# Kernel tuning notes

Hardware: AMD Instinct MI355X
Metric: run time of the kernel (lower is better)

## Reference

```python
import jax, jax.numpy as jnp
import numpy as np

N, E, G = 50000, 400000, 500
H, C, IN, ED = 4, 64, 9, 3
NEG = 0.2   # LeakyReLU negative slope (PyG GATv2 default)
EPS = 1e-5  # BatchNorm eps


def _gatv2(x, src, dst, ea, Wl, bl, Wr, We, att, bias):
    # PyG GATv2Conv, concat=False (mean over heads), eval mode (no dropout)
    xl = (x @ Wl + bl).reshape(-1, H, C)   # source transform  [N,H,C]
    xr = (x @ Wr).reshape(-1, H, C)        # target transform  [N,H,C]
    ee = (ea @ We).reshape(-1, H, C)       # edge transform    [E,H,C]
    m = xl[src] + xr[dst] + ee             # [E,H,C]
    s = jnp.einsum('ehc,hc->eh', jax.nn.leaky_relu(m, NEG), att)  # [E,H]
    smax = jax.ops.segment_max(s, dst, num_segments=N)
    ex = jnp.exp(s - smax[dst])
    den = jax.ops.segment_sum(ex, dst, num_segments=N)
    alpha = ex / den[dst]                  # segment softmax over in-edges of dst
    out = jax.ops.segment_sum(xl[src] * alpha[:, :, None], dst, num_segments=N)
    return out.mean(axis=1) + bias         # [N,C]


def _bn(x, g, b, mu, var):
    return (x - mu) * (g * jax.lax.rsqrt(var + EPS)) + b


def setup_inputs() -> dict:
    key = jax.random.key(0)
    ks = jax.random.split(key, 32)
    f = lambda k, s: (jax.random.normal(k, s, jnp.float32) * 0.1)
    inp = dict(
        x=jax.random.normal(ks[0], (N, IN), jnp.float32),
        edge_index=jax.random.randint(ks[1], (2, E), 0, N),
        batch=jnp.sort(jax.random.randint(ks[2], (N,), 0, G)),
        edge_attr=jax.random.normal(ks[3], (E, ED), jnp.float32),
        # input head conv (in=9)
        W0l=f(ks[4], (IN, H * C)), b0l=f(ks[5], (H * C,)),
        W0r=f(ks[6], (IN, H * C)), W0e=f(ks[7], (ED, H * C)),
        a0=f(ks[8], (H, C)), c0=f(ks[9], (C,)),
        # 3 residual conv layers (in=64), stacked
        Wl=f(ks[10], (3, C, H * C)), bl=f(ks[11], (3, H * C)),
        Wr=f(ks[12], (3, C, H * C)), We=f(ks[13], (3, ED, H * C)),
        a=f(ks[14], (3, H, C)), cb=f(ks[15], (3, C)),
        # 4 batchnorms (eval mode running stats)
        bn_g=jnp.ones((4, C), jnp.float32) + f(ks[16], (4, C)),
        bn_b=f(ks[17], (4, C)),
        bn_m=f(ks[18], (4, C)),
        bn_v=jnp.ones((4, C), jnp.float32),
        # output MLP head
        Wo1=f(ks[19], (C, C // 2)), bo1=f(ks[20], (C // 2,)),
        Wo2=f(ks[21], (C // 2, 1)), bo2=f(ks[22], (1,)),
    )
    return inp


def reference(x, edge_index, batch, edge_attr,
              W0l, b0l, W0r, W0e, a0, c0,
              Wl, bl, Wr, We, a, cb,
              bn_g, bn_b, bn_m, bn_v,
              Wo1, bo1, Wo2, bo2):
    src, dst = edge_index[0], edge_index[1]
    h = _gatv2(x, src, dst, edge_attr, W0l, b0l, W0r, W0e, a0, c0)
    h = jax.nn.elu(_bn(h, bn_g[0], bn_b[0], bn_m[0], bn_v[0]))
    for i in range(3):
        z = _gatv2(h, src, dst, edge_attr, Wl[i], bl[i], Wr[i], We[i], a[i], cb[i])
        z = jax.nn.elu(_bn(z, bn_g[i + 1], bn_b[i + 1], bn_m[i + 1], bn_v[i + 1]))
        h = h + z
    # global mean pool over graphs
    cnt = jax.ops.segment_sum(jnp.ones((N,), h.dtype), batch, num_segments=G)
    pooled = jax.ops.segment_sum(h, batch, num_segments=G) / jnp.maximum(cnt, 1.0)[:, None]
    hid = jax.nn.elu(pooled @ Wo1 + bo1)
    return hid @ Wo2 + bo2  # [G,1]
```

## Files before the change

kernel.cpp:

```cpp
#include <hip/hip_runtime.h>
#include <hip/hip_fp16.h>
#include <math.h>

typedef _Float16 h8 __attribute__((ext_vector_type(8)));
typedef float f4 __attribute__((ext_vector_type(4)));

__global__ __launch_bounds__(256) void count_kernel(const int* __restrict__ dst,
                                                    int* __restrict__ deg, int E) {
    int e = blockIdx.x * 256 + threadIdx.x;
    if (e < E) atomicAdd(&deg[dst[e]], 1);
}

#define SCAN_TPB 256
#define SCAN_VPT 4
#define SCAN_ELEMS (SCAN_TPB * SCAN_VPT)

__global__ __launch_bounds__(256) void scan_phase1(const int* __restrict__ deg,
                                                   int* __restrict__ bsum, int n) {
    __shared__ int sh[SCAN_TPB];
    int base = blockIdx.x * SCAN_ELEMS + threadIdx.x * SCAN_VPT;
    int s = 0;
#pragma unroll
    for (int j = 0; j < SCAN_VPT; j++) { int i = base + j; if (i < n) s += deg[i]; }
    sh[threadIdx.x] = s;
    __syncthreads();
    for (int off = 128; off; off >>= 1) {
        if (threadIdx.x < (unsigned)off) sh[threadIdx.x] += sh[threadIdx.x + off];
        __syncthreads();
    }
    if (threadIdx.x == 0) bsum[blockIdx.x] = sh[0];
}

__global__ __launch_bounds__(256) void scan_phase2(int* __restrict__ bsum, int nb,
                                                   int* __restrict__ rowptr, int n) {
    __shared__ int sh[256];
    int v = (threadIdx.x < (unsigned)nb) ? bsum[threadIdx.x] : 0;
    sh[threadIdx.x] = v;
    __syncthreads();
    for (int off = 1; off < 256; off <<= 1) {
        int t = (threadIdx.x >= (unsigned)off) ? sh[threadIdx.x - off] : 0;
        __syncthreads();
        sh[threadIdx.x] += t;
        __syncthreads();
    }
    if (threadIdx.x < (unsigned)nb) bsum[threadIdx.x] = sh[threadIdx.x] - v;
    if (threadIdx.x == 0) rowptr[n] = sh[255];
}

__global__ __launch_bounds__(256) void scan_phase3(const int* __restrict__ deg,
                                                   const int* __restrict__ bsum,
                                                   int* __restrict__ rowptr,
                                                   int* __restrict__ cursor, int n) {
    __shared__ int sh[SCAN_TPB];
    int tid = threadIdx.x;
    int base = blockIdx.x * SCAN_ELEMS + tid * SCAN_VPT;
    int v[SCAN_VPT];
    int s = 0;
#pragma unroll
    for (int j = 0; j < SCAN_VPT; j++) { int i = base + j; v[j] = (i < n) ? deg[i] : 0; s += v[j]; }
    sh[tid] = s;
    __syncthreads();
    for (int off = 1; off < SCAN_TPB; off <<= 1) {
        int t = (tid >= off) ? sh[tid - off] : 0;
        __syncthreads();
        sh[tid] += t;
        __syncthreads();
    }
    int ex = sh[tid] - s + bsum[blockIdx.x];
#pragma unroll
    for (int j = 0; j < SCAN_VPT; j++) {
        int i = base + j;
        if (i < n) { rowptr[i] = ex; cursor[i] = ex; ex += v[j]; }
    }
}

__global__ __launch_bounds__(256) void scatter_kernel(const int* __restrict__ src,
                                                      const int* __restrict__ dst,
                                                      const float* __restrict__ ea,
                                                      int* __restrict__ cursor,
                                                      float4* __restrict__ csr4, int E) {
    int e = blockIdx.x * 256 + threadIdx.x;
    if (e < E) {
        int d = dst[e];
        int pos = atomicAdd(&cursor[d], 1);
        size_t eb3 = (size_t)e * 3;
        csr4[pos] = make_float4(__int_as_float(src[e]), ea[eb3], ea[eb3 + 1], ea[eb3 + 2]);
    }
}

__global__ __launch_bounds__(256) void bnprep_kernel(const float* __restrict__ c0,
                                                     const float* __restrict__ cb,
                                                     const float* __restrict__ bng,
                                                     const float* __restrict__ bnb,
                                                     const float* __restrict__ bnm,
                                                     const float* __restrict__ bnv,
                                                     float* __restrict__ epi) {
    int t = threadIdx.x;
    int l = t >> 6, c = t & 63;
    float s = bng[l * 64 + c] * rsqrtf(bnv[l * 64 + c] + 1e-5f);
    float bias = (l == 0) ? c0[c] : cb[(l - 1) * 64 + c];
    epi[l * 128 + c] = 0.25f * s;
    epi[l * 128 + 64 + c] = (bias - bnm[l * 64 + c]) * s + bnb[l * 64 + c];
}

__global__ __launch_bounds__(256) void gstart_kernel(const int* __restrict__ batch,
                                                     int* __restrict__ gstart,
                                                     int Nn, int Gg) {
    int n = blockIdx.x * 256 + threadIdx.x;
    if (n >= Nn) return;
    int b = batch[n];
    int prev = (n == 0) ? -1 : batch[n - 1];
    for (int g = prev + 1; g <= b; g++) gstart[g] = n;
    if (n == Nn - 1)
        for (int g = b + 1; g <= Gg; g++) gstart[g] = Nn;
}

__global__ __launch_bounds__(256) void wprep_kernel(const float* __restrict__ W0l,
                                                    const float* __restrict__ W0r,
                                                    const float* __restrict__ Wl,
                                                    const float* __restrict__ Wr,
                                                    __half* __restrict__ Wp) {
    int t = blockIdx.x * 256 + threadIdx.x;
    int layer = t >> 12;
    int r = t & 4095;
    int lane = r & 63;
    int ks = (r >> 6) & 1;
    int gct = r >> 7;
    int K = (layer == 0) ? 9 : 64;
    const float* Wsrc;
    if (layer == 0) Wsrc = (gct < 16) ? W0l : W0r;
    else            Wsrc = ((gct < 16) ? Wl : Wr) + (size_t)(layer - 1) * 64 * 256;
    int cl = ((gct & 15) << 4) + (lane & 15);
    int k0 = (ks << 5) + ((lane >> 4) << 3);
    __half vals[8] __attribute__((aligned(16)));
#pragma unroll
    for (int j = 0; j < 8; j++) {
        int k = k0 + j;
        vals[j] = __float2half_rn((k < K) ? Wsrc[(size_t)k * 256 + cl] : 0.f);
    }
    *(uint4*)(Wp + (size_t)t * 8) = *(const uint4*)vals;
}

template <int K>
__global__ __launch_bounds__(256) void gemm2_mfma_kernel(const float* __restrict__ xin,
                                                         const __half* __restrict__ Wp,
                                                         const float* __restrict__ bl,
                                                         __half* __restrict__ xl,
                                                         __half* __restrict__ xr, int Nn) {
    constexpr int NKS = (K > 32) ? 2 : 1;
    constexpr int KP = NKS * 32;
    __shared__ __align__(16) float shx[32][KP + 4];
    int tid = threadIdx.x;
    int lane = tid & 63;
    int wv = tid >> 6;
    int nb = blockIdx.x * 32;
    int l15 = lane & 15;
    int lg = lane >> 4;

    if (K != KP) {
        for (int q = tid; q < 32 * KP; q += 256) shx[q / KP][q % KP] = 0.f;
        __syncthreads();
    }
    if (K == 64) {
        for (int q = tid; q < 32 * 16; q += 256) {
            int r = q >> 4, c4 = q & 15;
            int node = nb + r;
            float4 v = (node < Nn) ? *(const float4*)(xin + (size_t)node * 64 + c4 * 4)
                                   : make_float4(0.f, 0.f, 0.f, 0.f);
            *(float4*)&shx[r][c4 * 4] = v;
        }
    } else {
        for (int q = tid; q < 32 * K; q += 256) {
            int r = q / K, c = q - r * K;
            int node = nb + r;
            shx[r][c] = (node < Nn) ? xin[(size_t)node * K + c] : 0.f;
        }
    }
    __syncthreads();

    h8 afr[8][NKS];
#pragma unroll
    for (int i = 0; i < 8; i++) {
        int gct = wv * 8 + i;
#pragma unroll
        for (int ks = 0; ks < NKS; ks++)
            afr[i][ks] = *(const h8*)(Wp + (((size_t)(gct * 2 + ks)) * 64 + lane) * 8);
    }
    h8 bfr[2][NKS];
#pragma unroll
    for (int nt = 0; nt < 2; nt++) {
        int row = nt * 16 + l15;
#pragma unroll
        for (int ks = 0; ks < NKS; ks++) {
            int k0 = ks * 32 + lg * 8;
            float4 f0 = *(const float4*)&shx[row][k0];
            float4 f1 = *(const float4*)&shx[row][k0 + 4];
            h8 b;
            b[0] = (_Float16)f0.x; b[1] = (_Float16)f0.y;
            b[2] = (_Float16)f0.z; b[3] = (_Float16)f0.w;
            b[4] = (_Float16)f1.x; b[5] = (_Float16)f1.y;
            b[6] = (_Float16)f1.z; b[7] = (_Float16)f1.w;
            bfr[nt][ks] = b;
        }
    }
    f4 acc[8][2];
#pragma unroll
    for (int i = 0; i < 8; i++) {
        int gct = wv * 8 + i;
        f4 ini;
        if (gct < 16) {
            float4 b4 = *(const float4*)(bl + (gct << 4) + (lg << 2));
            ini[0] = b4.x; ini[1] = b4.y; ini[2] = b4.z; ini[3] = b4.w;
        } else {
            ini[0] = 0.f; ini[1] = 0.f; ini[2] = 0.f; ini[3] = 0.f;
        }
        acc[i][0] = ini;
        acc[i][1] = ini;
    }
#pragma unroll
    for (int i = 0; i < 8; i++)
#pragma unroll
        for (int nt = 0; nt < 2; nt++)
#pragma unroll
            for (int ks = 0; ks < NKS; ks++)
                acc[i][nt] = __builtin_amdgcn_mfma_f32_16x16x32_f16(
                    afr[i][ks], bfr[nt][ks], acc[i][nt], 0, 0, 0);
#pragma unroll
    for (int i = 0; i < 8; i++) {
        int gct = wv * 8 + i;
        __half* outp = (gct < 16) ? xl : xr;
        int cl = ((gct & 15) << 4) + (lg << 2);
#pragma unroll
        for (int nt = 0; nt < 2; nt++) {
            int node = nb + nt * 16 + l15;
            if (node < Nn) {
                __half h4[4] __attribute__((aligned(8)));
                h4[0] = __float2half_rn(acc[i][nt][0]);
                h4[1] = __float2half_rn(acc[i][nt][1]);
                h4[2] = __float2half_rn(acc[i][nt][2]);
                h4[3] = __float2half_rn(acc[i][nt][3]);
                *(uint2*)(outp + (size_t)node * 256 + cl) = *(const uint2*)h4;
            }
        }
    }
}

#define EB 6

#define GISSUE(S, ibase)                                                               \
    {                                                                                  \
        _Pragma("unroll") for (int j = 0; j < EB; j++) {                               \
            int idx = (ibase) + j;                                                     \
            if (idx < end) {                                                           \
                float4 ce = csr4[idx];                  \
                cey##S[j] = ce.y; cez##S[j] = ce.z; cew##S[j] = ce.w;                  \
                int sn = __float_as_int(ce.x);                                         \
                xpk##S[j] = *(const uint2*)(xl + ((size_t)sn << 8) + (lane << 2));     \
            } else {                                                                   \
                cey##S[j] = 0.f; cez##S[j] = 0.f; cew##S[j] = 0.f;                     \
                xpk##S[j] = make_uint2(0u, 0u);                                        \
            }                                                                          \
        }                                                                              \
    }

#define GCOMPUTE(S, ibase)                                                             \
    {                                                                                  \
        float p[EB];                                                                   \
        _Pragma("unroll") for (int j = 0; j < EB; j++) {                               \
            int idx = (ibase) + j;                                                     \
            if (idx < end) {                                                           \
                float2 f0 = __half22float2(*(const __half2*)&xpk##S[j].x);             \
                float2 f1 = __half22float2(*(const __half2*)&xpk##S[j].y);             \
                float tx = fmaf(cey##S[j], we0.x,                                      \
                             fmaf(cez##S[j], we1.x, fmaf(cew##S[j], we2.x, xr0.x)))    \
                           + f0.x;                                                     \
                float ty = fmaf(cey##S[j], we0.y,                                      \
                             fmaf(cez##S[j], we1.y, fmaf(cew##S[j], we2.y, xr0.y)))    \
                           + f0.y;                                                     \
                float tz = fmaf(cey##S[j], we0.z,                                      \
                             fmaf(cez##S[j], we1.z, fmaf(cew##S[j], we2.z, xr1.x)))    \
                           + f1.x;                                                     \
                float tw = fmaf(cey##S[j], we0.w,                                      \
                             fmaf(cez##S[j], we1.w, fmaf(cew##S[j], we2.w, xr1.y)))    \
                           + f1.y;                                                     \
                float pp = tx * (tx > 0.f ? attv.x : att02.x);                         \
                pp = fmaf(ty, (ty > 0.f ? attv.y : att02.y), pp);                      \
                pp = fmaf(tz, (tz > 0.f ? attv.z : att02.z), pp);                      \
                pp = fmaf(tw, (tw > 0.f ? attv.w : att02.w), pp);                      \
                p[j] = pp;                                                             \
            } else p[j] = -INFINITY;                                                   \
        }                                                                              \
        _Pragma("unroll") for (int off = 1; off < 16; off <<= 1) {                     \
            _Pragma("unroll") for (int j = 0; j < EB; j++) p[j] += __shfl_xor(p[j], off); \
        }                                                                              \
        _Pragma("unroll") for (int j = 0; j < EB; j++) {                               \
            float wv2 = __expf(p[j]);                                                  \
            float2 f0 = __half22float2(*(const __half2*)&xpk##S[j].x);                 \
            float2 f1 = __half22float2(*(const __half2*)&xpk##S[j].y);                 \
            acc.x = fmaf(wv2, f0.x, acc.x);                                            \
            acc.y = fmaf(wv2, f0.y, acc.y);                                            \
            acc.z = fmaf(wv2, f1.x, acc.z);                                            \
            acc.w = fmaf(wv2, f1.y, acc.w);                                            \
            l_run += wv2;                                                              \
        }                                                                              \
    }

__global__ __launch_bounds__(256) void gat_kernel(const __half* __restrict__ xl,
                                                  const __half* __restrict__ xr,
                                                  const float* __restrict__ We,
                                                  const float* __restrict__ att,
                                                  const float* __restrict__ epi,
                                                  const int* __restrict__ rowptr,
                                                  const float4* __restrict__ csr4,
                                                  float* __restrict__ hout,
                                                  const float* __restrict__ hres,
                                                  int Nn) {
    int tid = threadIdx.x;
    int lane = tid & 63;
    int w = __builtin_amdgcn_readfirstlane(tid >> 6);
    int wave = blockIdx.x * 4 + w;
    int nwaves = gridDim.x * 4;

    float4 we0 = *(const float4*)&We[lane * 4];
    float4 we1 = *(const float4*)&We[256 + lane * 4];
    float4 we2 = *(const float4*)&We[512 + lane * 4];
    float4 attv = *(const float4*)&att[lane * 4];
    float4 att02 = make_float4(0.2f * attv.x, 0.2f * attv.y, 0.2f * attv.z, 0.2f * attv.w);
    float4 eA = *(const float4*)&epi[(lane & 15) * 4];
    float4 eB4 = *(const float4*)&epi[64 + (lane & 15) * 4];

    int d = wave;
    if (d >= Nn) return;
    int beg = rowptr[d];
    int end = rowptr[d + 1];
    uint2 xrp = *(const uint2*)(xr + ((size_t)d << 8) + (lane << 2));

    uint2 xpkA[EB], xpkB[EB];
    float ceyA[EB], cezA[EB], cewA[EB], ceyB[EB], cezB[EB], cewB[EB];

    while (d < Nn) {
        int dn = d + nwaves;
        int begn = 0, endn = 0;
        uint2 xrpn = make_uint2(0u, 0u);
        if (dn < Nn) {
            begn = rowptr[dn];
            endn = rowptr[dn + 1];
            xrpn = *(const uint2*)(xr + ((size_t)dn << 8) + (lane << 2));
        }
        float2 xr0 = __half22float2(*(const __half2*)&xrp.x);
        float2 xr1 = __half22float2(*(const __half2*)&xrp.y);

        float l_run = 0.f;
        float4 acc = make_float4(0.f, 0.f, 0.f, 0.f);

        int i = beg;
        if (i < end) {
            GISSUE(A, i);
            for (;;) {
                int nx = i + EB;
                if (nx < end) GISSUE(B, nx);
                GCOMPUTE(A, i);
                i = nx;
                if (i >= end) break;
                nx = i + EB;
                if (nx < end) GISSUE(A, nx);
                GCOMPUTE(B, i);
                i = nx;
                if (i >= end) break;
            }
        }
        float inv = (end > beg) ? 1.f / l_run : 0.f;
        float4 o = make_float4(acc.x * inv, acc.y * inv, acc.z * inv, acc.w * inv);
#pragma unroll
        for (int off = 16; off < 64; off <<= 1) {
            o.x += __shfl_xor(o.x, off);
            o.y += __shfl_xor(o.y, off);
            o.z += __shfl_xor(o.z, off);
            o.w += __shfl_xor(o.w, off);
        }
        if (lane < 16) {
            float vx = fmaf(o.x, eA.x, eB4.x);
            float vy = fmaf(o.y, eA.y, eB4.y);
            float vz = fmaf(o.z, eA.z, eB4.z);
            float vw = fmaf(o.w, eA.w, eB4.w);
            vx = vx > 0.f ? vx : expm1f(vx);
            vy = vy > 0.f ? vy : expm1f(vy);
            vz = vz > 0.f ? vz : expm1f(vz);
            vw = vw > 0.f ? vw : expm1f(vw);
            if (hres) {
                float4 r4 = *(const float4*)&hres[((size_t)d << 6) + (lane << 2)];
                vx += r4.x; vy += r4.y; vz += r4.z; vw += r4.w;
            }
            *(float4*)&hout[((size_t)d << 6) + (lane << 2)] = make_float4(vx, vy, vz, vw);
        }
        d = dn; beg = begn; end = endn; xrp = xrpn;
    }
}

__global__ __launch_bounds__(256) void pool_kernel(const float* __restrict__ h,
                                                   const int* __restrict__ gstart,
                                                   float* __restrict__ pooled, int Gg) {
    __shared__ float red[4][64];
    int g = blockIdx.x;
    int tid = threadIdx.x;
    int lane = tid & 63, w = tid >> 6;
    int gs = gstart[g], ge = gstart[g + 1];
    float s = 0.f;
    for (int n = gs + w; n < ge; n += 4) s += h[((size_t)n << 6) + lane];
    red[w][lane] = s;
    __syncthreads();
    if (tid < 64) {
        float tot = red[0][tid] + red[1][tid] + red[2][tid] + red[3][tid];
        float c = fmaxf((float)(ge - gs), 1.f);
        pooled[((size_t)g << 6) + tid] = tot / c;
    }
}

__global__ __launch_bounds__(64) void head_kernel(const float* __restrict__ pooled,
                                                  const float* __restrict__ Wo1,
                                                  const float* __restrict__ bo1,
                                                  const float* __restrict__ Wo2,
                                                  const float* __restrict__ bo2,
                                                  float* __restrict__ out, int Gg) {
    int g = blockIdx.x;
    int t = threadIdx.x;
    __shared__ float sp[64];
    sp[t] = pooled[(size_t)g * 64 + t];
    __syncthreads();
    float hid = 0.f;
    if (t < 32) {
        hid = bo1[t];
        for (int k = 0; k < 64; k++) hid += sp[k] * Wo1[k * 32 + t];
        hid = hid > 0.f ? hid : expm1f(hid);
        hid *= Wo2[t];
    }
#pragma unroll
    for (int off = 32; off; off >>= 1) hid += __shfl_xor(hid, off);
    if (t == 0) out[g] = hid + bo2[0];
}

extern "C" void kernel_launch(void* const* d_in, const int* in_sizes, int n_in,
                              void* d_out, int out_size, void* d_ws, size_t ws_size,
                              hipStream_t stream) {
    const float* x   = (const float*)d_in[0];
    const int*   ei  = (const int*)d_in[1];
    const int*   bat = (const int*)d_in[2];
    const float* ea  = (const float*)d_in[3];
    const float* W0l = (const float*)d_in[4];
    const float* b0l = (const float*)d_in[5];
    const float* W0r = (const float*)d_in[6];
    const float* W0e = (const float*)d_in[7];
    const float* a0  = (const float*)d_in[8];
    const float* c0  = (const float*)d_in[9];
    const float* Wl  = (const float*)d_in[10];
    const float* bl  = (const float*)d_in[11];
    const float* Wr  = (const float*)d_in[12];
    const float* We  = (const float*)d_in[13];
    const float* a   = (const float*)d_in[14];
    const float* cb  = (const float*)d_in[15];
    const float* bng = (const float*)d_in[16];
    const float* bnb = (const float*)d_in[17];
    const float* bnm = (const float*)d_in[18];
    const float* bnv = (const float*)d_in[19];
    const float* Wo1 = (const float*)d_in[20];
    const float* bo1 = (const float*)d_in[21];
    const float* Wo2 = (const float*)d_in[22];
    const float* bo2 = (const float*)d_in[23];

    int Nn = in_sizes[2];
    int Ee = in_sizes[1] / 2;
    int Gg = out_size;
    const int* srcv = ei;
    const int* dstv = ei + Ee;

    char* w = (char*)d_ws;
    auto alloc = [&](size_t bytes) {
        char* p = w;
        w += (bytes + 255) & ~(size_t)255;
        return p;
    };
    __half* xlb    = (__half*)alloc((size_t)Nn * 256 * 2);
    __half* xrb    = (__half*)alloc((size_t)Nn * 256 * 2);
    float*  hbuf   = (float*)alloc((size_t)Nn * 64 * 4);
    int*    deg    = (int*)alloc((size_t)Nn * 4);
    int*    rowptr = (int*)alloc((size_t)(Nn + 1) * 4);
    int*    cursor = (int*)alloc((size_t)Nn * 4);
    float4* csr4   = (float4*)alloc((size_t)Ee * 16);
    float*  pooled = (float*)alloc((size_t)Gg * 64 * 4);
    int*    gstart = (int*)alloc((size_t)(Gg + 1) * 4);
    int*    bsum   = (int*)alloc(256 * 4);
    float*  epi    = (float*)alloc(4 * 128 * 4);
    __half* Wp     = (__half*)alloc((size_t)4 * 32768 * 2);

    int nscan = (Nn + SCAN_ELEMS - 1) / SCAN_ELEMS;

    hipMemsetAsync(deg, 0, (size_t)Nn * 4, stream);
    count_kernel<<<(Ee + 255) / 256, 256, 0, stream>>>(dstv, deg, Ee);
    scan_phase1<<<nscan, 256, 0, stream>>>(deg, bsum, Nn);
    scan_phase2<<<1, 256, 0, stream>>>(bsum, nscan, rowptr, Nn);
    scan_phase3<<<nscan, 256, 0, stream>>>(deg, bsum, rowptr, cursor, Nn);
    scatter_kernel<<<(Ee + 255) / 256, 256, 0, stream>>>(srcv, dstv, ea, cursor, csr4, Ee);
    bnprep_kernel<<<1, 256, 0, stream>>>(c0, cb, bng, bnb, bnm, bnv, epi);
    wprep_kernel<<<64, 256, 0, stream>>>(W0l, W0r, Wl, Wr, Wp);
    gstart_kernel<<<(Nn + 255) / 256, 256, 0, stream>>>(bat, gstart, Nn, Gg);

    int gatg = 2048;
    int gemg = (Nn + 31) / 32;

    gemm2_mfma_kernel<9><<<gemg, 256, 0, stream>>>(x, Wp, b0l, xlb, xrb, Nn);
    gat_kernel<<<gatg, 256, 0, stream>>>(xlb, xrb, W0e, a0, epi,
                                         rowptr, csr4, hbuf, nullptr, Nn);
    for (int i = 0; i < 3; i++) {
        gemm2_mfma_kernel<64><<<gemg, 256, 0, stream>>>(
            hbuf, Wp + (size_t)(i + 1) * 32768, bl + (size_t)i * 256, xlb, xrb, Nn);
        gat_kernel<<<gatg, 256, 0, stream>>>(
            xlb, xrb, We + (size_t)i * 768, a + (size_t)i * 256, epi + (size_t)(i + 1) * 128,
            rowptr, csr4, hbuf, hbuf, Nn);
    }

    pool_kernel<<<Gg, 256, 0, stream>>>(hbuf, gstart, pooled, Gg);
    head_kernel<<<Gg, 64, 0, stream>>>(pooled, Wo1, bo1, Wo2, bo2, (float*)d_out, Gg);
}
```

Measured before the change: 425.8 us.

## Balance GAT node ranges across waves by edge count using rowptr binary search

Adds a small kernel that splits the destination nodes into 8192 contiguous ranges holding roughly equal numbers of edges, found by binary search over rowptr. Each GAT wave now walks its own contiguous range instead of striding by the total wave count. This evens out per-wave work and makes neighbouring destination nodes share a wave, which may improve locality. The cost is one extra tiny launch, and a wave can end up with many low-degree nodes handled one after another.

```diff
diff --git a/kernel.cpp b/kernel.cpp
--- a/kernel.cpp
+++ b/kernel.cpp
@@ -4,6 +4,8 @@
 
 typedef _Float16 h8 __attribute__((ext_vector_type(8)));
 typedef float f4 __attribute__((ext_vector_type(4)));
+
+#define NWAVES 8192
 
 __global__ __launch_bounds__(256) void count_kernel(const int* __restrict__ dst,
                                                     int* __restrict__ deg, int E) {
@@ -86,6 +88,22 @@
         size_t eb3 = (size_t)e * 3;
         csr4[pos] = make_float4(__int_as_float(src[e]), ea[eb3], ea[eb3 + 1], ea[eb3 + 2]);
     }
+}
+
+__global__ __launch_bounds__(256) void wbal_kernel(const int* __restrict__ rowptr,
+                                                   int Nn, int* __restrict__ wstart) {
+    int q = blockIdx.x * 256 + threadIdx.x;
+    if (q > NWAVES) return;
+    if (q == 0) { wstart[0] = 0; return; }
+    if (q == NWAVES) { wstart[NWAVES] = Nn; return; }
+    int Etot = rowptr[Nn];
+    int t = (int)(((long long)q * Etot) / NWAVES);
+    int lo = 0, hi = Nn;
+    while (lo < hi) {
+        int mid = (lo + hi) >> 1;
+        if (rowptr[mid] < t) lo = mid + 1; else hi = mid;
+    }
+    wstart[q] = lo;
 }
 
 __global__ __launch_bounds__(256) void bnprep_kernel(const float* __restrict__ c0,
@@ -311,6 +329,7 @@
                                                   const float* __restrict__ att,
                                                   const float* __restrict__ epi,
                                                   const int* __restrict__ rowptr,
+                                                  const int* __restrict__ wstart,
                                                   const float4* __restrict__ csr4,
                                                   float* __restrict__ hout,
                                                   const float* __restrict__ hres,
@@ -319,7 +338,6 @@
     int lane = tid & 63;
     int w = __builtin_amdgcn_readfirstlane(tid >> 6);
     int wave = blockIdx.x * 4 + w;
-    int nwaves = gridDim.x * 4;
 
     float4 we0 = *(const float4*)&We[lane * 4];
     float4 we1 = *(const float4*)&We[256 + lane * 4];
@@ -329,8 +347,9 @@
     float4 eA = *(const float4*)&epi[(lane & 15) * 4];
     float4 eB4 = *(const float4*)&epi[64 + (lane & 15) * 4];
 
-    int d = wave;
-    if (d >= Nn) return;
+    int ns = wstart[wave], ne = wstart[wave + 1];
+    int d = ns;
+    if (d >= ne) return;
     int beg = rowptr[d];
     int end = rowptr[d + 1];
     uint2 xrp = *(const uint2*)(xr + ((size_t)d << 8) + (lane << 2));
@@ -338,11 +357,11 @@
     uint2 xpkA[EB], xpkB[EB];
     float ceyA[EB], cezA[EB], cewA[EB], ceyB[EB], cezB[EB], cewB[EB];
 
-    while (d < Nn) {
-        int dn = d + nwaves;
+    while (d < ne) {
+        int dn = d + 1;
         int begn = 0, endn = 0;
         uint2 xrpn = make_uint2(0u, 0u);
-        if (dn < Nn) {
+        if (dn < ne) {
             begn = rowptr[dn];
             endn = rowptr[dn + 1];
             xrpn = *(const uint2*)(xr + ((size_t)dn << 8) + (lane << 2));
@@ -488,6 +507,7 @@
     float4* csr4   = (float4*)alloc((size_t)Ee * 16);
     float*  pooled = (float*)alloc((size_t)Gg * 64 * 4);
     int*    gstart = (int*)alloc((size_t)(Gg + 1) * 4);
+    int*    wstart = (int*)alloc((size_t)(NWAVES + 1) * 4);
     int*    bsum   = (int*)alloc(256 * 4);
     float*  epi    = (float*)alloc(4 * 128 * 4);
     __half* Wp     = (__half*)alloc((size_t)4 * 32768 * 2);
@@ -500,22 +520,23 @@
     scan_phase2<<<1, 256, 0, stream>>>(bsum, nscan, rowptr, Nn);
     scan_phase3<<<nscan, 256, 0, stream>>>(deg, bsum, rowptr, cursor, Nn);
     scatter_kernel<<<(Ee + 255) / 256, 256, 0, stream>>>(srcv, dstv, ea, cursor, csr4, Ee);
+    wbal_kernel<<<(NWAVES + 256) / 256, 256, 0, stream>>>(rowptr, Nn, wstart);
     bnprep_kernel<<<1, 256, 0, stream>>>(c0, cb, bng, bnb, bnm, bnv, epi);
     wprep_kernel<<<64, 256, 0, stream>>>(W0l, W0r, Wl, Wr, Wp);
     gstart_kernel<<<(Nn + 255) / 256, 256, 0, stream>>>(bat, gstart, Nn, Gg);
 
-    int gatg = 2048;
+    int gatg = NWAVES / 4;
     int gemg = (Nn + 31) / 32;
 
     gemm2_mfma_kernel<9><<<gemg, 256, 0, stream>>>(x, Wp, b0l, xlb, xrb, Nn);
     gat_kernel<<<gatg, 256, 0, stream>>>(xlb, xrb, W0e, a0, epi,
-                                         rowptr, csr4, hbuf, nullptr, Nn);
+                                         rowptr, wstart, csr4, hbuf, nullptr, Nn);
     for (int i = 0; i < 3; i++) {
         gemm2_mfma_kernel<64><<<gemg, 256, 0, stream>>>(
             hbuf, Wp + (size_t)(i + 1) * 32768, bl + (size_t)i * 256, xlb, xrb, Nn);
         gat_kernel<<<gatg, 256, 0, stream>>>(
             xlb, xrb, We + (size_t)i * 768, a + (size_t)i * 256, epi + (size_t)(i + 1) * 128,
-            rowptr, csr4, hbuf, hbuf, Nn);
+            rowptr, wstart, csr4, hbuf, hbuf, Nn);
     }
 
     pool_kernel<<<Gg, 256, 0, stream>>>(hbuf, gstart, pooled, Gg);
```

Result: no change. 426.4 us (+0.1%).
